# Optimization experiments

Measured on AMD Instinct MI355X. Metric: run time of the kernel, lower is better.

The kernel has to match this reference:

```python
import jax, jax.numpy as jnp
import numpy as np

B, S, D, V = 512, 64, 128, 256
NH = 4                 # sLSTM heads
HD = D // NH           # 32
INNER = 2 * D          # mLSTM inner dim (proj_factor=2.0)
NHM = 4                # mLSTM heads
DHM = INNER // NHM     # 64
BS = 4                 # qkv_proj_blocksize
NB = INNER // BS       # 64 block-diagonal qkv blocks
K = 4                  # causal conv kernel
FF = D                 # gated FFN up dim (proj_factor=1.0)


def setup_inputs():
    key = jax.random.key(0)
    ks = iter(jax.random.split(key, 40))
    def rn(shape, scale=0.02):
        return jax.random.normal(next(ks), shape, dtype=jnp.float32) * scale
    return {
        "x": jax.random.randint(next(ks), (B, S), 0, V, dtype=jnp.int32),
        "embed": rn((V, D), 0.02),
        "s_ln1": jnp.ones((2, D), jnp.float32),
        "s_gates_w": rn((2, 4, NH, HD, HD), 0.08),   # i,f,z,o headwise input projections
        "s_rec": rn((2, 4, NH, HD, HD), 0.08),       # block-diagonal recurrent kernels
        "s_bias": rn((2, 4, NH, HD), 0.1),
        "s_gn": jnp.ones((2, D), jnp.float32),
        "s_ln2": jnp.ones((2, D), jnp.float32),
        "s_ff_up": rn((2, D, 2 * FF), 0.05),
        "s_ff_down": rn((2, FF, D), 0.05),
        "m_ln1": jnp.ones((2, D), jnp.float32),
        "m_up": rn((2, D, 2 * INNER), 0.05),
        "m_conv_w": rn((2, INNER, K), 0.1),
        "m_conv_b": jnp.zeros((2, INNER), jnp.float32),
        "m_qkv_w": rn((2, 3, NB, BS, BS), 0.2),
        "m_ig_w": rn((2, 3 * INNER, NHM), 0.02),
        "m_ig_b": jnp.zeros((2, NHM), jnp.float32),
        "m_fg_w": rn((2, 3 * INNER, NHM), 0.02),
        "m_fg_b": 3.0 * jnp.ones((2, NHM), jnp.float32),
        "m_skip": jnp.ones((2, INNER), jnp.float32),
        "m_onorm": jnp.ones((2, INNER), jnp.float32),
        "m_down": rn((2, INNER, D), 0.05),
        "m_ln2": jnp.ones((2, D), jnp.float32),
        "m_ff_up": rn((2, D, 2 * FF), 0.05),
        "m_ff_down": rn((2, FF, D), 0.05),
        "post_ln": jnp.ones((D,), jnp.float32),
        "head_w": rn((D, V), 0.05),
        "head_b": jnp.zeros((V,), jnp.float32),
    }


def _ln(x, w, eps=1e-5):
    mu = x.mean(-1, keepdims=True)
    var = x.var(-1, keepdims=True)
    return (x - mu) * jax.lax.rsqrt(var + eps) * w


def _mh_ln(xh, w, eps=1e-5):
    # xh: [B,S,nh,dh]; per-head layernorm (GroupNorm), weight-only affine
    mu = xh.mean(-1, keepdims=True)
    var = xh.var(-1, keepdims=True)
    y = (xh - mu) * jax.lax.rsqrt(var + eps)
    return y * w.reshape(xh.shape[-2], xh.shape[-1])


def _ffn(x, up, down):
    g, u = jnp.split(x @ up, 2, axis=-1)
    return (jax.nn.gelu(g) * u) @ down


def _slstm(x, gw, rw, bias, gn):
    # vanilla sLSTM: stabilized exp-gated scalar-memory recurrence, block-diag recurrent kernels
    Bq, Sq, Dq = x.shape
    xh = x.reshape(Bq, Sq, NH, HD)
    # precompute input contributions for all 4 gates: [S,B,4,NH,HD]
    gx = jnp.einsum('bsnd,gned->sbgne', xh, gw) + bias

    def step(carry, g):
        h, c, n, m = carry
        raw = g + jnp.einsum('bnd,gned->bgne', h, rw)
        i_r, f_r, z_r, o_r = raw[:, 0], raw[:, 1], raw[:, 2], raw[:, 3]
        logfplusm = m + jax.nn.log_sigmoid(f_r)
        m_new = jnp.maximum(i_r, logfplusm)
        i = jnp.exp(i_r - m_new)
        f = jnp.exp(logfplusm - m_new)
        c_new = f * c + i * jnp.tanh(z_r)
        n_new = f * n + i
        h_new = jax.nn.sigmoid(o_r) * c_new / n_new
        return (h_new, c_new, n_new, m_new), h_new

    z0 = jnp.zeros((Bq, NH, HD), x.dtype)
    _, ys = jax.lax.scan(step, (z0, z0, z0, z0), gx)
    y = jnp.transpose(ys, (1, 0, 2, 3))  # [B,S,NH,HD]
    return _mh_ln(y, gn).reshape(Bq, Sq, Dq)


def _mlstm(x, up, cw, cb, qkvw, igw, igb, fgw, fgb, skip, onw, down):
    # pre-up-projection mLSTM layer with parallel stabilized matrix-memory cell
    Bq, Sq, _ = x.shape
    xm, z = jnp.split(x @ up, 2, axis=-1)  # [B,S,INNER] each
    # causal depthwise conv + swish
    conv = jax.lax.conv_general_dilated(
        xm.transpose(0, 2, 1), cw[:, None, :],
        window_strides=(1,), padding=[(K - 1, 0)], feature_group_count=INNER)
    x_conv = jax.nn.silu(conv.transpose(0, 2, 1) + cb)

    def hw(t, w):  # block-diagonal (headwise) linear, w: [NB, out, in]
        th = t.reshape(Bq, Sq, NB, BS)
        return jnp.einsum('bsni,noi->bsno', th, w).reshape(Bq, Sq, INNER)

    q = hw(x_conv, qkvw[0])
    k = hw(x_conv, qkvw[1])
    v = hw(xm, qkvw[2])

    gate_in = jnp.concatenate([q, k, v], axis=-1)          # [B,S,3*INNER]
    ig = (gate_in @ igw + igb).transpose(0, 2, 1)          # [B,NHM,S]
    fg = (gate_in @ fgw + fgb).transpose(0, 2, 1)

    qh = q.reshape(Bq, Sq, NHM, DHM).transpose(0, 2, 1, 3)  # [B,NHM,S,DHM]
    kh = k.reshape(Bq, Sq, NHM, DHM).transpose(0, 2, 1, 3)
    vh = v.reshape(Bq, Sq, NHM, DHM).transpose(0, 2, 1, 3)

    log_f = jax.nn.log_sigmoid(fg)                          # [B,NHM,S]
    c = jnp.concatenate([jnp.zeros_like(log_f[..., :1]), jnp.cumsum(log_f, -1)], -1)
    mat = c[..., 1:, None] - c[..., None, 1:]               # (i,j): sum_{t=j+1..i} log f_t
    mask = jnp.tril(jnp.ones((Sq, Sq), bool))
    log_D = jnp.where(mask, mat, -jnp.inf) + ig[..., None, :]
    max_log_D = jnp.max(log_D, -1, keepdims=True)           # [B,NHM,S,1]
    Dm = jnp.exp(log_D - max_log_D)
    qk = jnp.einsum('bhid,bhjd->bhij', qh, kh) * (DHM ** -0.5)
    Cm = qk * Dm
    norm = jnp.maximum(jnp.abs(Cm.sum(-1, keepdims=True)), jnp.exp(-max_log_D))
    Cn = Cm / (norm + 1e-6)
    h = jnp.einsum('bhij,bhjd->bhid', Cn, vh).transpose(0, 2, 1, 3)  # [B,S,NHM,DHM]
    h = _mh_ln(h, onw).reshape(Bq, Sq, INNER)
    h = (h + skip * x_conv) * jax.nn.silu(z)
    return h @ down


def _forward(x, embed, s_ln1, s_gates_w, s_rec, s_bias, s_gn, s_ln2, s_ff_up, s_ff_down,
             m_ln1, m_up, m_conv_w, m_conv_b, m_qkv_w, m_ig_w, m_ig_b, m_fg_w, m_fg_b,
             m_skip, m_onorm, m_down, m_ln2, m_ff_up, m_ff_down, post_ln, head_w, head_b):
    h = embed[x]  # [B,S,D]
    for i in range(2):
        # sLSTM block (even positions 0, 2)
        h = h + _slstm(_ln(h, s_ln1[i]), s_gates_w[i], s_rec[i], s_bias[i], s_gn[i])
        h = h + _ffn(_ln(h, s_ln2[i]), s_ff_up[i], s_ff_down[i])
        # mLSTM block (odd positions 1, 3)
        h = h + _mlstm(_ln(h, m_ln1[i]), m_up[i], m_conv_w[i], m_conv_b[i], m_qkv_w[i],
                       m_ig_w[i], m_ig_b[i], m_fg_w[i], m_fg_b[i], m_skip[i], m_onorm[i], m_down[i])
        h = h + _ffn(_ln(h, m_ln2[i]), m_ff_up[i], m_ff_down[i])
    h = _ln(h, post_ln)
    return h @ head_w + head_b


def reference(x, embed, s_ln1, s_gates_w, s_rec, s_bias, s_gn, s_ln2, s_ff_up, s_ff_down,
              m_ln1, m_up, m_conv_w, m_conv_b, m_qkv_w, m_ig_w, m_ig_b, m_fg_w, m_fg_b,
              m_skip, m_onorm, m_down, m_ln2, m_ff_up, m_ff_down, post_ln, head_w, head_b):
    return _forward(x, embed, s_ln1, s_gates_w, s_rec, s_bias, s_gn, s_ln2, s_ff_up, s_ff_down,
                    m_ln1, m_up, m_conv_w, m_conv_b, m_qkv_w, m_ig_w, m_ig_b, m_fg_w, m_fg_b,
                    m_skip, m_onorm, m_down, m_ln2, m_ff_up, m_ff_down, post_ln, head_w, head_b)
```

## Files before the change

### kernel.cpp

```cpp
#include <hip/hip_runtime.h>
#include <math.h>


__device__ __forceinline__ float sigf(float x){ return 1.f/(1.f+__expf(-x)); }
__device__ __forceinline__ float siluf(float x){ return x/(1.f+__expf(-x)); }
__device__ __forceinline__ float logsigf(float x){ return fminf(x,0.f) - log1pf(__expf(-fabsf(x))); }
__device__ __forceinline__ float geluf(float x){
  return 0.5f*x*(1.f+tanhf(0.7978845608028654f*(x+0.044715f*x*x*x)));
}
__device__ __forceinline__ void sums4(float4 v, float& s, float& q){
  s += v.x+v.y+v.z+v.w;
  q += v.x*v.x+v.y*v.y+v.z*v.z+v.w*v.w;
}

__device__ __forceinline__ void ln_rows(const float* __restrict__ src, const float* __restrict__ lnw,
                                        float* __restrict__ dst, int dstride,
                                        float (*red)[8], float (*red2)[8], int t)
{
  int r = t >> 3, l8 = t & 7;
  const float4* s4 = (const float4*)(src + (size_t)r*128 + l8*16);
  float4 v0=s4[0], v1=s4[1], v2=s4[2], v3=s4[3];
  float su=0.f, sq=0.f;
  sums4(v0,su,sq); sums4(v1,su,sq); sums4(v2,su,sq); sums4(v3,su,sq);
  red[r][l8]=su; red2[r][l8]=sq;
  __syncthreads();
  float ts=0.f, tq=0.f;
  #pragma unroll
  for (int k=0;k<8;k++){ ts+=red[r][k]; tq+=red2[r][k]; }
  float mu = ts*(1.f/128.f);
  float var = tq*(1.f/128.f) - mu*mu;
  float iv = rsqrtf(var+1e-5f);
  int c0 = l8*16;
  float vv[16];
  *(float4*)&vv[0]=v0; *(float4*)&vv[4]=v1; *(float4*)&vv[8]=v2; *(float4*)&vv[12]=v3;
  #pragma unroll
  for (int q2=0;q2<16;q2++) dst[r*dstride + c0 + q2] = (vv[q2]-mu)*iv*lnw[c0+q2];
}

__global__ __launch_bounds__(256) void k_embed(const int* __restrict__ x, const float* __restrict__ embed,
                                               float* __restrict__ h)
{
  int idx4 = blockIdx.x*256 + threadIdx.x;
  int tok = idx4 >> 5;
  int c4  = idx4 & 31;
  int id = x[tok];
  reinterpret_cast<float4*>(h)[idx4] = reinterpret_cast<const float4*>(embed)[id*32 + c4];
}

__global__ __launch_bounds__(512) void k_prep(
    const float* __restrict__ qkvw,
    const float* __restrict__ igw,
    const float* __restrict__ fgw,
    float* __restrict__ wtab)
{
  int t = threadIdx.x;
  int l = t >> 8, c = t & 255;
  int nb = c >> 2, i = c & 3;
  const float* qk  = qkvw + l*3072;
  const float* igl = igw + l*3072;
  const float* fgl = fgw + l*3072;
  float igc[4]={0,0,0,0}, igm[4]={0,0,0,0}, fgc[4]={0,0,0,0}, fgm[4]={0,0,0,0};
  #pragma unroll
  for (int o=0;o<4;o++){
    float wq = qk[nb*16 + o*4 + i];
    float wk = qk[1024 + nb*16 + o*4 + i];
    float wv = qk[2048 + nb*16 + o*4 + i];
    int no = nb*4+o;
    #pragma unroll
    for (int m=0;m<4;m++){
      igc[m] += wq*igl[no*4+m] + wk*igl[(256+no)*4+m];
      igm[m] += wv*igl[(512+no)*4+m];
      fgc[m] += wq*fgl[no*4+m] + wk*fgl[(256+no)*4+m];
      fgm[m] += wv*fgl[(512+no)*4+m];
    }
  }
  float* dst = wtab + l*4096;
  #pragma unroll
  for (int m=0;m<4;m++){
    dst[(0*256+c)*4+m] = igc[m];
    dst[(1*256+c)*4+m] = igm[m];
    dst[(2*256+c)*4+m] = fgc[m];
    dst[(3*256+c)*4+m] = fgm[m];
  }
}

__global__ __launch_bounds__(512) void k_slstm(
    float* __restrict__ h, const float* __restrict__ lnw,
    const float* __restrict__ gw, const float* __restrict__ rw,
    const float* __restrict__ bias, const float* __restrict__ gn)
{
  __shared__ float xh[64][128];
  __shared__ float hb[128];
  __shared__ float raw[512];
  __shared__ float red[64][8];
  __shared__ float red2[64][8];
  __shared__ float mu_s[64][4];
  __shared__ float iv_s[64][4];

  int t = threadIdx.x;
  int b = blockIdx.x;
  float* hrow = h + (size_t)b*8192;

  ln_rows(hrow, lnw, &xh[0][0], 128, red, red2, t);
  __syncthreads();

  int g  = t >> 7;
  int nh = (t >> 5) & 3;
  int e  = t & 31;
  float wg[32], wr[32];
  {
    const float4* g4 = (const float4*)(gw + (((g*4+nh)*32+e)*32));
    const float4* r4 = (const float4*)(rw + (((g*4+nh)*32+e)*32));
    #pragma unroll
    for (int q=0;q<8;q++){
      float4 a=g4[q]; wg[4*q]=a.x; wg[4*q+1]=a.y; wg[4*q+2]=a.z; wg[4*q+3]=a.w;
      float4 c=r4[q]; wr[4*q]=c.x; wr[4*q+1]=c.y; wr[4*q+2]=c.z; wr[4*q+3]=c.w;
    }
  }
  float bs = bias[(g*4+nh)*32+e];
  float c_s=0.f, n_s=0.f, m_s=0.f;
  if (t<128) hb[t]=0.f;
  __syncthreads();

  for (int s=0;s<64;s++){
    const float4* xr = (const float4*)&xh[s][nh*32];
    const float4* hr = (const float4*)&hb[nh*32];
    float acc = bs;
    #pragma unroll
    for (int q=0;q<8;q++){
      float4 xv = xr[q]; float4 hv = hr[q];
      acc += xv.x*wg[4*q+0] + xv.y*wg[4*q+1] + xv.z*wg[4*q+2] + xv.w*wg[4*q+3];
      acc += hv.x*wr[4*q+0] + hv.y*wr[4*q+1] + hv.z*wr[4*q+2] + hv.w*wr[4*q+3];
    }
    raw[t] = acc;
    __syncthreads();
    if (t < 128){
      float i_r = raw[t], f_r = raw[128+t], z_r = raw[256+t], o_r = raw[384+t];
      float lf = m_s + logsigf(f_r);
      float mn = fmaxf(i_r, lf);
      float iv = __expf(i_r-mn), fv = __expf(lf-mn);
      c_s = fv*c_s + iv*tanhf(z_r);
      n_s = fv*n_s + iv;
      m_s = mn;
      float hn = sigf(o_r)*c_s/n_s;
      hb[t] = hn;
      xh[s][t] = hn;
    }
    __syncthreads();
  }

  if (t < 256){
    int s = t>>2, n = t&3;
    const float4* yr = (const float4*)&xh[s][n*32];
    float su=0.f, sq=0.f;
    #pragma unroll
    for (int q=0;q<8;q++){ float4 v = yr[q]; sums4(v,su,sq); }
    float mu = su*(1.f/32.f);
    float var = sq*(1.f/32.f) - mu*mu;
    mu_s[s][n]=mu; iv_s[s][n]=rsqrtf(var+1e-5f);
  }
  __syncthreads();
  #pragma unroll
  for (int rr=0; rr<16; rr++){
    int idx = t + 512*rr;
    int s = idx>>7, c = idx&127;
    float y = (xh[s][c] - mu_s[s][c>>5]) * iv_s[s][c>>5] * gn[c];
    hrow[idx] += y;
  }
}

__global__ __launch_bounds__(256) void k_ffn(
    float* __restrict__ h, const float* __restrict__ lnw,
    const float* __restrict__ up, const float* __restrict__ down)
{
  __shared__ float xln[32][132];
  __shared__ float hid[32][132];
  __shared__ float bws[2][16][256];
  __shared__ float red[32][8];
  __shared__ float red2[32][8];
  int t = threadIdx.x;
  size_t tok0 = (size_t)blockIdx.x * 32;

  ln_rows(h + tok0*128, lnw, &xln[0][0], 132, red, red2, t);
  __syncthreads();

  int r0 = (t >> 5) * 4;
  int c0 = (t & 31) * 4;

  {
    float4 regs[4];
    auto stage = [&](int kc){
      #pragma unroll
      for (int j=0;j<4;j++){
        int idx = t + 256*j;
        int row = idx >> 6, c4 = idx & 63;
        regs[j] = *(const float4*)(up + (size_t)(kc*16+row)*256 + c4*4);
      }
    };
    auto wrt = [&](int buf){
      #pragma unroll
      for (int j=0;j<4;j++){
        int idx = t + 256*j;
        int row = idx >> 6, c4 = idx & 63;
        *(float4*)&bws[buf][row][c4*4] = regs[j];
      }
    };
    stage(0); wrt(0);
    __syncthreads();
    float4 ag[4], au[4];
    #pragma unroll
    for (int i=0;i<4;i++){ ag[i]=make_float4(0,0,0,0); au[i]=make_float4(0,0,0,0); }
    for (int kc=0;kc<8;kc++){
      if (kc<7) stage(kc+1);
      int buf = kc & 1;
      #pragma unroll
      for (int k=0;k<16;k++){
        float4 wg = *(float4*)&bws[buf][k][c0];
        float4 wu = *(float4*)&bws[buf][k][c0+128];
        int kk = kc*16 + k;
        #pragma unroll
        for (int i=0;i<4;i++){
          float xv = xln[r0+i][kk];
          ag[i].x+=xv*wg.x; ag[i].y+=xv*wg.y; ag[i].z+=xv*wg.z; ag[i].w+=xv*wg.w;
          au[i].x+=xv*wu.x; au[i].y+=xv*wu.y; au[i].z+=xv*wu.z; au[i].w+=xv*wu.w;
        }
      }
      if (kc<7) wrt(buf^1);
      __syncthreads();
    }
    #pragma unroll
    for (int i=0;i<4;i++){
      hid[r0+i][c0+0] = geluf(ag[i].x)*au[i].x;
      hid[r0+i][c0+1] = geluf(ag[i].y)*au[i].y;
      hid[r0+i][c0+2] = geluf(ag[i].z)*au[i].z;
      hid[r0+i][c0+3] = geluf(ag[i].w)*au[i].w;
    }
  }
  __syncthreads();

  {
    float (*bw2)[16][128] = (float (*)[16][128])bws;
    float4 regs[2];
    auto stage = [&](int kc){
      #pragma unroll
      for (int j=0;j<2;j++){
        int idx = t + 256*j;
        int row = idx >> 5, c4 = idx & 31;
        regs[j] = *(const float4*)(down + (size_t)(kc*16+row)*128 + c4*4);
      }
    };
    auto wrt = [&](int buf){
      #pragma unroll
      for (int j=0;j<2;j++){
        int idx = t + 256*j;
        int row = idx >> 5, c4 = idx & 31;
        *(float4*)&bw2[buf][row][c4*4] = regs[j];
      }
    };
    stage(0); wrt(0);
    __syncthreads();
    float4 a2[4];
    #pragma unroll
    for (int i=0;i<4;i++) a2[i]=make_float4(0,0,0,0);
    for (int kc=0;kc<8;kc++){
      if (kc<7) stage(kc+1);
      int buf = kc & 1;
      #pragma unroll
      for (int k=0;k<16;k++){
        float4 wv = *(float4*)&bw2[buf][k][c0];
        int kk = kc*16 + k;
        #pragma unroll
        for (int i=0;i<4;i++){
          float xv = hid[r0+i][kk];
          a2[i].x+=xv*wv.x; a2[i].y+=xv*wv.y; a2[i].z+=xv*wv.z; a2[i].w+=xv*wv.w;
        }
      }
      if (kc<7) wrt(buf^1);
      __syncthreads();
    }
    #pragma unroll
    for (int i=0;i<4;i++){
      float* dstp = h + (tok0 + r0 + i)*128 + c0;
      float4 hv = *(float4*)dstp;
      hv.x += a2[i].x; hv.y += a2[i].y; hv.z += a2[i].z; hv.w += a2[i].w;
      *(float4*)dstp = hv;
    }
  }
}

__global__ __launch_bounds__(256) void k_up(
    const float* __restrict__ h, const float* __restrict__ lnw,
    const float* __restrict__ up, float* __restrict__ xm, float* __restrict__ z)
{
  __shared__ float xln[64][132];
  __shared__ float bw[2][32][128];
  __shared__ float red[64][4];
  __shared__ float red2[64][4];
  int t = threadIdx.x;
  int mt = blockIdx.x >> 2, nt = blockIdx.x & 3;
  size_t tok0 = (size_t)mt * 64;
  int n0 = nt * 128;

  {
    int r = t >> 2, l = t & 3;
    const float4* s4 = (const float4*)(h + (tok0 + (size_t)r)*128 + l*32);
    float4 v[8];
    float su=0.f, sq=0.f;
    #pragma unroll
    for (int q=0;q<8;q++){ v[q]=s4[q]; sums4(v[q],su,sq); }
    red[r][l]=su; red2[r][l]=sq;
    __syncthreads();
    float ts=red[r][0]+red[r][1]+red[r][2]+red[r][3];
    float tq=red2[r][0]+red2[r][1]+red2[r][2]+red2[r][3];
    float mu=ts*(1.f/128.f);
    float var=tq*(1.f/128.f)-mu*mu;
    float iv=rsqrtf(var+1e-5f);
    int cb=l*32;
    #pragma unroll
    for (int q=0;q<8;q++){
      xln[r][cb+q*4+0]=(v[q].x-mu)*iv*lnw[cb+q*4+0];
      xln[r][cb+q*4+1]=(v[q].y-mu)*iv*lnw[cb+q*4+1];
      xln[r][cb+q*4+2]=(v[q].z-mu)*iv*lnw[cb+q*4+2];
      xln[r][cb+q*4+3]=(v[q].w-mu)*iv*lnw[cb+q*4+3];
    }
  }

  float4 regs[4];
  auto stage = [&](int kc){
    #pragma unroll
    for (int j=0;j<4;j++){
      int idx = t + 256*j;
      int row = idx >> 5, c4 = idx & 31;
      regs[j] = *(const float4*)(up + (size_t)(kc*32+row)*512 + n0 + c4*4);
    }
  };
  auto wrt = [&](int buf){
    #pragma unroll
    for (int j=0;j<4;j++){
      int idx = t + 256*j;
      int row = idx >> 5, c4 = idx & 31;
      *(float4*)&bw[buf][row][c4*4] = regs[j];
    }
  };
  stage(0); wrt(0);
  __syncthreads();

  int r0 = (t >> 5) * 8;
  int c0 = (t & 31) * 4;
  float4 acc4[8];
  #pragma unroll
  for (int i=0;i<8;i++) acc4[i]=make_float4(0,0,0,0);

  for (int kc=0;kc<4;kc++){
    if (kc<3) stage(kc+1);
    int buf = kc & 1;
    #pragma unroll 8
    for (int k=0;k<32;k++){
      float4 wv = *(float4*)&bw[buf][k][c0];
      int kk = kc*32 + k;
      #pragma unroll
      for (int i=0;i<8;i++){
        float xv = xln[r0+i][kk];
        acc4[i].x += xv*wv.x; acc4[i].y += xv*wv.y; acc4[i].z += xv*wv.z; acc4[i].w += xv*wv.w;
      }
    }
    if (kc<3) wrt(buf^1);
    __syncthreads();
  }

  float* dst; int cbase;
  if (n0 < 256){ dst = xm; cbase = n0 + c0; }
  else         { dst = z;  cbase = n0 - 256 + c0; }
  #pragma unroll
  for (int i=0;i<8;i++)
    *(float4*)(dst + (tok0 + r0 + i)*256 + cbase) = acc4[i];
}

__global__ __launch_bounds__(256) void k_convgates(
    const float* __restrict__ xm, float* __restrict__ xc,
    const float* __restrict__ cw, const float* __restrict__ cb,
    const float* __restrict__ wtab,
    const float* __restrict__ igb, const float* __restrict__ fgb,
    float* __restrict__ ig, float* __restrict__ fg)
{
  int t = threadIdx.x;
  int b = blockIdx.x;
  int c4 = t & 63, sr = t >> 6;
  int c0 = c4*4;
  const float* src = xm + (size_t)b*16384;
  float* dstc = xc + (size_t)b*16384;

  float4 r0 = *(const float4*)(cw + (c0+0)*4);
  float4 r1 = *(const float4*)(cw + (c0+1)*4);
  float4 r2 = *(const float4*)(cw + (c0+2)*4);
  float4 r3 = *(const float4*)(cw + (c0+3)*4);
  float4 wk0 = make_float4(r0.x, r1.x, r2.x, r3.x);
  float4 wk1 = make_float4(r0.y, r1.y, r2.y, r3.y);
  float4 wk2 = make_float4(r0.z, r1.z, r2.z, r3.z);
  float4 wk3 = make_float4(r0.w, r1.w, r2.w, r3.w);
  float4 bias4 = *(const float4*)(cb + c0);

  float4 Wigc[4], Wigm[4], Wfgc[4], Wfgm[4];
  #pragma unroll
  for (int i=0;i<4;i++){
    Wigc[i] = *(const float4*)(wtab + (0*256+c0+i)*4);
    Wigm[i] = *(const float4*)(wtab + (1*256+c0+i)*4);
    Wfgc[i] = *(const float4*)(wtab + (2*256+c0+i)*4);
    Wfgm[i] = *(const float4*)(wtab + (3*256+c0+i)*4);
  }

  int s0 = sr*16;
  float4 w0 = make_float4(0,0,0,0), w1 = w0, w2 = w0;
  if (s0 >= 3){
    w0 = *(const float4*)(src + (size_t)(s0-3)*256 + c0);
    w1 = *(const float4*)(src + (size_t)(s0-2)*256 + c0);
    w2 = *(const float4*)(src + (size_t)(s0-1)*256 + c0);
  }

  for (int j=0;j<16;j++){
    int s = s0 + j;
    float4 w3 = *(const float4*)(src + (size_t)s*256 + c0);
    float4 a;
    a.x = bias4.x + w0.x*wk0.x + w1.x*wk1.x + w2.x*wk2.x + w3.x*wk3.x;
    a.y = bias4.y + w0.y*wk0.y + w1.y*wk1.y + w2.y*wk2.y + w3.y*wk3.y;
    a.z = bias4.z + w0.z*wk0.z + w1.z*wk1.z + w2.z*wk2.z + w3.z*wk3.z;
    a.w = bias4.w + w0.w*wk0.w + w1.w*wk1.w + w2.w*wk2.w + w3.w*wk3.w;
    a.x = siluf(a.x); a.y = siluf(a.y); a.z = siluf(a.z); a.w = siluf(a.w);
    *(float4*)(dstc + (size_t)s*256 + c0) = a;

    float pig[4] = {0.f,0.f,0.f,0.f};
    float pfg[4] = {0.f,0.f,0.f,0.f};
    const float xcv[4] = {a.x,a.y,a.z,a.w};
    const float xmv[4] = {w3.x,w3.y,w3.z,w3.w};
    #pragma unroll
    for (int i=0;i<4;i++){
      pig[0] += xcv[i]*Wigc[i].x + xmv[i]*Wigm[i].x;
      pig[1] += xcv[i]*Wigc[i].y + xmv[i]*Wigm[i].y;
      pig[2] += xcv[i]*Wigc[i].z + xmv[i]*Wigm[i].z;
      pig[3] += xcv[i]*Wigc[i].w + xmv[i]*Wigm[i].w;
      pfg[0] += xcv[i]*Wfgc[i].x + xmv[i]*Wfgm[i].x;
      pfg[1] += xcv[i]*Wfgc[i].y + xmv[i]*Wfgm[i].y;
      pfg[2] += xcv[i]*Wfgc[i].z + xmv[i]*Wfgm[i].z;
      pfg[3] += xcv[i]*Wfgc[i].w + xmv[i]*Wfgm[i].w;
    }
    #pragma unroll
    for (int off=32; off>=1; off>>=1){
      #pragma unroll
      for (int m=0;m<4;m++){
        pig[m] += __shfl_xor(pig[m], off, 64);
        pfg[m] += __shfl_xor(pfg[m], off, 64);
      }
    }
    if (c4 == 0){
      #pragma unroll
      for (int m=0;m<4;m++){
        ig[(size_t)b*256 + m*64 + s] = pig[m] + igb[m];
        fg[(size_t)b*256 + m*64 + s] = pfg[m] + fgb[m];
      }
    }
    w0=w1; w1=w2; w2=w3;
  }
}

__global__ __launch_bounds__(256) void k_attn(
    float* __restrict__ xm, const float* __restrict__ xc,
    const float* __restrict__ qkvw,
    const float* __restrict__ igp, const float* __restrict__ fgp,
    const float* __restrict__ onorm)
{
  __shared__ float qs[64][68];
  __shared__ float ksm[64][68];
  __shared__ float vsm[64][68];
  __shared__ float xcl[64][68];
  __shared__ float xml[64][68];
  __shared__ float cnm[64][65];
  __shared__ float csum[65];
  __shared__ float pmax[64];
  __shared__ float igl[64];
  __shared__ float lfs[64];
  __shared__ float nrec[64];

  int t = threadIdx.x;
  int b = blockIdx.x >> 2, hh = blockIdx.x & 3;
  const float* xcb = xc + (size_t)b*16384 + hh*64;
  float* xmb = xm + (size_t)b*16384 + hh*64;

  #pragma unroll
  for (int j=0;j<4;j++){
    int u = t + 256*j;
    int r = u >> 4, q4 = u & 15;
    *(float4*)&xcl[r][q4*4] = *(const float4*)(xcb + (size_t)r*256 + q4*4);
    *(float4*)&xml[r][q4*4] = *(const float4*)(xmb + (size_t)r*256 + q4*4);
  }
  if (t < 64){
    lfs[t] = logsigf(fgp[(size_t)b*256 + hh*64 + t]);
    igl[t] = igp[(size_t)b*256 + hh*64 + t];
  }
  __syncthreads();
  if (t == 0){
    float cacc = 0.f, pm = -1e30f;
    csum[0] = 0.f;
    for (int s=0;s<64;s++){
      cacc += lfs[s];
      csum[s+1] = cacc;
      pm = fmaxf(pm, igl[s] - cacc);
      pmax[s] = pm;
    }
  }
  #pragma unroll
  for (int j=0;j<4;j++){
    int u = t + 256*j;
    int s = u >> 4, lb = u & 15;
    int nb = hh*16 + lb;
    const float* xq = &xcl[s][lb*4];
    const float* xv = &xml[s][lb*4];
    #pragma unroll
    for (int o=0;o<4;o++){
      float4 wq = *(const float4*)(qkvw + nb*16 + o*4);
      float4 wkk = *(const float4*)(qkvw + 1024 + nb*16 + o*4);
      float4 wv = *(const float4*)(qkvw + 2048 + nb*16 + o*4);
      qs[s][lb*4+o]  = wq.x*xq[0]+wq.y*xq[1]+wq.z*xq[2]+wq.w*xq[3];
      ksm[s][lb*4+o] = wkk.x*xq[0]+wkk.y*xq[1]+wkk.z*xq[2]+wkk.w*xq[3];
      vsm[s][lb*4+o] = wv.x*xv[0]+wv.y*xv[1]+wv.z*xv[2]+wv.w*xv[3];
    }
  }
  __syncthreads();

  int i = t >> 2;
  int jq = t & 3;
  float mi = csum[i+1] + pmax[i];
  float rs = 0.f;
  for (int jj=0;jj<16;jj++){
    int j = jq*16 + jj;
    if (j <= i){
      const float4* qa = (const float4*)&qs[i][0];
      const float4* ka = (const float4*)&ksm[j][0];
      float dp = 0.f;
      #pragma unroll
      for (int kk=0;kk<16;kk++){
        float4 a = qa[kk], c = ka[kk];
        dp += a.x*c.x + a.y*c.y + a.z*c.z + a.w*c.w;
      }
      float val = dp * 0.125f * __expf(csum[i+1] - csum[j+1] + igl[j] - mi);
      cnm[i][j] = val;
      rs += val;
    }
  }
  rs += __shfl_xor(rs, 1, 4);
  rs += __shfl_xor(rs, 2, 4);
  if (jq == 0){
    float nm = fmaxf(fabsf(rs), __expf(-mi));
    nrec[i] = 1.f/(nm + 1e-6f);
  }
  __syncthreads();

  int d0 = jq*16;
  float acc[16];
  #pragma unroll
  for (int q=0;q<16;q++) acc[q]=0.f;
  float nr = nrec[i];
  for (int j=0;j<=i;j++){
    float cwv = cnm[i][j] * nr;
    const float4* va = (const float4*)&vsm[j][d0];
    #pragma unroll
    for (int q=0;q<4;q++){
      float4 v4 = va[q];
      acc[q*4+0] += cwv*v4.x; acc[q*4+1] += cwv*v4.y; acc[q*4+2] += cwv*v4.z; acc[q*4+3] += cwv*v4.w;
    }
  }
  float su=0.f, sq=0.f;
  #pragma unroll
  for (int q=0;q<16;q++){ su += acc[q]; sq += acc[q]*acc[q]; }
  su += __shfl_xor(su,1,4); su += __shfl_xor(su,2,4);
  sq += __shfl_xor(sq,1,4); sq += __shfl_xor(sq,2,4);
  float mu = su*(1.f/64.f);
  float var = sq*(1.f/64.f) - mu*mu;
  float ivr = rsqrtf(var + 1e-5f);
  const float* onw = onorm + hh*64 + d0;
  #pragma unroll
  for (int q=0;q<4;q++){
    float4 o4;
    o4.x = (acc[q*4+0]-mu)*ivr*onw[q*4+0];
    o4.y = (acc[q*4+1]-mu)*ivr*onw[q*4+1];
    o4.z = (acc[q*4+2]-mu)*ivr*onw[q*4+2];
    o4.w = (acc[q*4+3]-mu)*ivr*onw[q*4+3];
    *(float4*)(xmb + (size_t)i*256 + d0 + q*4) = o4;
  }
}

__global__ __launch_bounds__(256) void k_comb_down(
    float* __restrict__ h, const float* __restrict__ hln,
    const float* __restrict__ xc, const float* __restrict__ z,
    const float* __restrict__ skip, const float* __restrict__ down)
{
  __shared__ float comb[32][260];
  __shared__ float bw[2][16][128];
  int t = threadIdx.x;
  size_t tok0 = (size_t)blockIdx.x*32;
  #pragma unroll
  for (int j=0;j<8;j++){
    int f4 = t + 256*j;
    int r = f4 >> 6, c4 = f4 & 63;
    size_t gi = (tok0 + r)*256 + c4*4;
    float4 a  = *(const float4*)(hln + gi);
    float4 xv = *(const float4*)(xc + gi);
    float4 zv = *(const float4*)(z + gi);
    float4 sk = *(const float4*)(skip + c4*4);
    float4 o;
    o.x = (a.x + sk.x*xv.x)*siluf(zv.x);
    o.y = (a.y + sk.y*xv.y)*siluf(zv.y);
    o.z = (a.z + sk.z*xv.z)*siluf(zv.z);
    o.w = (a.w + sk.w*xv.w)*siluf(zv.w);
    *(float4*)&comb[r][c4*4] = o;
  }

  float4 regs[2];
  auto stage = [&](int kc){
    #pragma unroll
    for (int j=0;j<2;j++){
      int idx = t + 256*j;
      int row = idx >> 5, c4 = idx & 31;
      regs[j] = *(const float4*)(down + (size_t)(kc*16+row)*128 + c4*4);
    }
  };
  auto wrt = [&](int buf){
    #pragma unroll
    for (int j=0;j<2;j++){
      int idx = t + 256*j;
      int row = idx >> 5, c4 = idx & 31;
      *(float4*)&bw[buf][row][c4*4] = regs[j];
    }
  };
  stage(0); wrt(0);
  __syncthreads();

  int r0 = (t >> 5) * 4;
  int c0 = (t & 31) * 4;
  float4 a2[4];
  #pragma unroll
  for (int i=0;i<4;i++) a2[i]=make_float4(0,0,0,0);
  for (int kc=0;kc<16;kc++){
    if (kc<15) stage(kc+1);
    int buf = kc & 1;
    #pragma unroll
    for (int k=0;k<16;k++){
      float4 wv = *(float4*)&bw[buf][k][c0];
      int kk = kc*16 + k;
      #pragma unroll
      for (int i=0;i<4;i++){
        float xv = comb[r0+i][kk];
        a2[i].x+=xv*wv.x; a2[i].y+=xv*wv.y; a2[i].z+=xv*wv.z; a2[i].w+=xv*wv.w;
      }
    }
    if (kc<15) wrt(buf^1);
    __syncthreads();
  }
  #pragma unroll
  for (int i=0;i<4;i++){
    float* dstp = h + (tok0 + r0 + i)*128 + c0;
    float4 hv = *(float4*)dstp;
    hv.x += a2[i].x; hv.y += a2[i].y; hv.z += a2[i].z; hv.w += a2[i].w;
    *(float4*)dstp = hv;
  }
}

__global__ __launch_bounds__(256) void k_head(
    const float* __restrict__ h, const float* __restrict__ lnw,
    const float* __restrict__ w, const float* __restrict__ bias2,
    float* __restrict__ out)
{
  __shared__ float xln[32][132];
  __shared__ float bws[2][16][256];
  __shared__ float red[32][8];
  __shared__ float red2[32][8];
  int t = threadIdx.x;
  size_t tok0 = (size_t)blockIdx.x * 32;

  ln_rows(h + tok0*128, lnw, &xln[0][0], 132, red, red2, t);
  __syncthreads();

  float4 regs[4];
  auto stage = [&](int kc){
    #pragma unroll
    for (int j=0;j<4;j++){
      int idx = t + 256*j;
      int row = idx >> 6, c4 = idx & 63;
      regs[j] = *(const float4*)(w + (size_t)(kc*16+row)*256 + c4*4);
    }
  };
  auto wrt = [&](int buf){
    #pragma unroll
    for (int j=0;j<4;j++){
      int idx = t + 256*j;
      int row = idx >> 6, c4 = idx & 63;
      *(float4*)&bws[buf][row][c4*4] = regs[j];
    }
  };
  stage(0); wrt(0);
  __syncthreads();

  int r0 = (t >> 5) * 4;
  int c0 = (t & 31) * 8;
  float4 a0[4], a1[4];
  #pragma unroll
  for (int i=0;i<4;i++){ a0[i]=make_float4(0,0,0,0); a1[i]=make_float4(0,0,0,0); }
  for (int kc=0;kc<8;kc++){
    if (kc<7) stage(kc+1);
    int buf = kc & 1;
    #pragma unroll
    for (int k=0;k<16;k++){
      float4 w0 = *(float4*)&bws[buf][k][c0];
      float4 w1 = *(float4*)&bws[buf][k][c0+4];
      int kk = kc*16 + k;
      #pragma unroll
      for (int i=0;i<4;i++){
        float xv = xln[r0+i][kk];
        a0[i].x+=xv*w0.x; a0[i].y+=xv*w0.y; a0[i].z+=xv*w0.z; a0[i].w+=xv*w0.w;
        a1[i].x+=xv*w1.x; a1[i].y+=xv*w1.y; a1[i].z+=xv*w1.z; a1[i].w+=xv*w1.w;
      }
    }
    if (kc<7) wrt(buf^1);
    __syncthreads();
  }
  float4 b0 = *(const float4*)(bias2 + c0);
  float4 b1 = *(const float4*)(bias2 + c0 + 4);
  #pragma unroll
  for (int i=0;i<4;i++){
    float* dstp = out + (tok0 + r0 + i)*256 + c0;
    float4 o0, o1;
    o0.x=a0[i].x+b0.x; o0.y=a0[i].y+b0.y; o0.z=a0[i].z+b0.z; o0.w=a0[i].w+b0.w;
    o1.x=a1[i].x+b1.x; o1.y=a1[i].y+b1.y; o1.z=a1[i].z+b1.z; o1.w=a1[i].w+b1.w;
    ((float4*)dstp)[0]=o0; ((float4*)dstp)[1]=o1;
  }
}

extern "C" void kernel_launch(void* const* d_in, const int* in_sizes, int n_in,
                              void* d_out, int out_size, void* d_ws, size_t ws_size,
                              hipStream_t stream)
{
  const int*   x      = (const int*)  d_in[0];
  const float* embed  = (const float*)d_in[1];
  const float* s_ln1  = (const float*)d_in[2];
  const float* s_gw   = (const float*)d_in[3];
  const float* s_rec  = (const float*)d_in[4];
  const float* s_bias = (const float*)d_in[5];
  const float* s_gn   = (const float*)d_in[6];
  const float* s_ln2  = (const float*)d_in[7];
  const float* s_ffu  = (const float*)d_in[8];
  const float* s_ffd  = (const float*)d_in[9];
  const float* m_ln1  = (const float*)d_in[10];
  const float* m_up   = (const float*)d_in[11];
  const float* m_cw   = (const float*)d_in[12];
  const float* m_cb   = (const float*)d_in[13];
  const float* m_qkv  = (const float*)d_in[14];
  const float* m_igw  = (const float*)d_in[15];
  const float* m_igb  = (const float*)d_in[16];
  const float* m_fgw  = (const float*)d_in[17];
  const float* m_fgb  = (const float*)d_in[18];
  const float* m_skip = (const float*)d_in[19];
  const float* m_onw  = (const float*)d_in[20];
  const float* m_down = (const float*)d_in[21];
  const float* m_ln2  = (const float*)d_in[22];
  const float* m_ffu  = (const float*)d_in[23];
  const float* m_ffd  = (const float*)d_in[24];
  const float* postln = (const float*)d_in[25];
  const float* headw  = (const float*)d_in[26];
  const float* headb  = (const float*)d_in[27];

  float* p = (float*)d_ws;
  float* hbuf = p; p += 4194304;
  size_t avail = ws_size / 4;
  const size_t need_full = 4194304ULL + 3ULL*8388608ULL + 2ULL*131072ULL + 8192ULL;
  float* xmbuf;
  if (avail >= need_full){ xmbuf = p; p += 8388608; }
  else                   { xmbuf = (float*)d_out; }
  float* zbuf  = p; p += 8388608;
  float* xcbuf = p; p += 8388608;
  float* igbuf = p; p += 131072;
  float* fgbuf = p; p += 131072;
  float* wtab  = p; p += 8192;

  k_prep<<<1, 512, 0, stream>>>(m_qkv, m_igw, m_fgw, wtab);
  k_embed<<<4096, 256, 0, stream>>>(x, embed, hbuf);

  for (int i=0;i<2;i++){
    k_slstm<<<512, 512, 0, stream>>>(hbuf, s_ln1+i*128, s_gw+i*16384, s_rec+i*16384,
                                     s_bias+i*512, s_gn+i*128);
    k_ffn<<<1024, 256, 0, stream>>>(hbuf, s_ln2+i*128, s_ffu+i*32768, s_ffd+i*16384);
    k_up<<<2048, 256, 0, stream>>>(hbuf, m_ln1+i*128, m_up+i*65536, xmbuf, zbuf);
    k_convgates<<<512, 256, 0, stream>>>(xmbuf, xcbuf, m_cw+i*1024, m_cb+i*256,
                                         wtab+i*4096, m_igb+i*4, m_fgb+i*4,
                                         igbuf, fgbuf);
    k_attn<<<2048, 256, 0, stream>>>(xmbuf, xcbuf, m_qkv+i*3072, igbuf, fgbuf, m_onw+i*256);
    k_comb_down<<<1024, 256, 0, stream>>>(hbuf, xmbuf, xcbuf, zbuf, m_skip+i*256, m_down+i*32768);
    k_ffn<<<1024, 256, 0, stream>>>(hbuf, m_ln2+i*128, m_ffu+i*32768, m_ffd+i*16384);
  }

  k_head<<<1024, 256, 0, stream>>>(hbuf, postln, headw, headb, (float*)d_out);
}
```

Baseline: 1.349 ms.

## Drop x staging in attention, hoist qkv weights and q row into registers

```diff
diff --git a/kernel.cpp b/kernel.cpp
--- a/kernel.cpp
+++ b/kernel.cpp
@@ -471,8 +471,6 @@
   __shared__ float qs[64][68];
   __shared__ float ksm[64][68];
   __shared__ float vsm[64][68];
-  __shared__ float xcl[64][68];
-  __shared__ float xml[64][68];
   __shared__ float cnm[64][65];
   __shared__ float csum[65];
   __shared__ float pmax[64];
@@ -485,18 +483,22 @@
   const float* xcb = xc + (size_t)b*16384 + hh*64;
   float* xmb = xm + (size_t)b*16384 + hh*64;
 
-  #pragma unroll
-  for (int j=0;j<4;j++){
-    int u = t + 256*j;
-    int r = u >> 4, q4 = u & 15;
-    *(float4*)&xcl[r][q4*4] = *(const float4*)(xcb + (size_t)r*256 + q4*4);
-    *(float4*)&xml[r][q4*4] = *(const float4*)(xmb + (size_t)r*256 + q4*4);
-  }
   if (t < 64){
     lfs[t] = logsigf(fgp[(size_t)b*256 + hh*64 + t]);
     igl[t] = igp[(size_t)b*256 + hh*64 + t];
   }
   __syncthreads();
+
+  int lb = t & 15;
+  int nb = hh*16 + lb;
+  float4 wq[4], wk[4], wv[4];
+  #pragma unroll
+  for (int o=0;o<4;o++){
+    wq[o] = *(const float4*)(qkvw + nb*16 + o*4);
+    wk[o] = *(const float4*)(qkvw + 1024 + nb*16 + o*4);
+    wv[o] = *(const float4*)(qkvw + 2048 + nb*16 + o*4);
+  }
+
   if (t == 0){
     float cacc = 0.f, pm = -1e30f;
     csum[0] = 0.f;
@@ -507,38 +509,49 @@
       pmax[s] = pm;
     }
   }
+
   #pragma unroll
   for (int j=0;j<4;j++){
-    int u = t + 256*j;
-    int s = u >> 4, lb = u & 15;
-    int nb = hh*16 + lb;
-    const float* xq = &xcl[s][lb*4];
-    const float* xv = &xml[s][lb*4];
-    #pragma unroll
-    for (int o=0;o<4;o++){
-      float4 wq = *(const float4*)(qkvw + nb*16 + o*4);
-      float4 wkk = *(const float4*)(qkvw + 1024 + nb*16 + o*4);
-      float4 wv = *(const float4*)(qkvw + 2048 + nb*16 + o*4);
-      qs[s][lb*4+o]  = wq.x*xq[0]+wq.y*xq[1]+wq.z*xq[2]+wq.w*xq[3];
-      ksm[s][lb*4+o] = wkk.x*xq[0]+wkk.y*xq[1]+wkk.z*xq[2]+wkk.w*xq[3];
-      vsm[s][lb*4+o] = wv.x*xv[0]+wv.y*xv[1]+wv.z*xv[2]+wv.w*xv[3];
-    }
+    int s = (t >> 4) + j*16;
+    float4 x4 = *(const float4*)(xcb + (size_t)s*256 + lb*4);
+    float4 m4 = *(const float4*)(xmb + (size_t)s*256 + lb*4);
+    float4 qv, kv, vv;
+    qv.x = wq[0].x*x4.x + wq[0].y*x4.y + wq[0].z*x4.z + wq[0].w*x4.w;
+    qv.y = wq[1].x*x4.x + wq[1].y*x4.y + wq[1].z*x4.z + wq[1].w*x4.w;
+    qv.z = wq[2].x*x4.x + wq[2].y*x4.y + wq[2].z*x4.z + wq[2].w*x4.w;
+    qv.w = wq[3].x*x4.x + wq[3].y*x4.y + wq[3].z*x4.z + wq[3].w*x4.w;
+    kv.x = wk[0].x*x4.x + wk[0].y*x4.y + wk[0].z*x4.z + wk[0].w*x4.w;
+    kv.y = wk[1].x*x4.x + wk[1].y*x4.y + wk[1].z*x4.z + wk[1].w*x4.w;
+    kv.z = wk[2].x*x4.x + wk[2].y*x4.y + wk[2].z*x4.z + wk[2].w*x4.w;
+    kv.w = wk[3].x*x4.x + wk[3].y*x4.y + wk[3].z*x4.z + wk[3].w*x4.w;
+    vv.x = wv[0].x*m4.x + wv[0].y*m4.y + wv[0].z*m4.z + wv[0].w*m4.w;
+    vv.y = wv[1].x*m4.x + wv[1].y*m4.y + wv[1].z*m4.z + wv[1].w*m4.w;
+    vv.z = wv[2].x*m4.x + wv[2].y*m4.y + wv[2].z*m4.z + wv[2].w*m4.w;
+    vv.w = wv[3].x*m4.x + wv[3].y*m4.y + wv[3].z*m4.z + wv[3].w*m4.w;
+    *(float4*)&qs[s][lb*4]  = qv;
+    *(float4*)&ksm[s][lb*4] = kv;
+    *(float4*)&vsm[s][lb*4] = vv;
   }
   __syncthreads();
 
   int i = t >> 2;
   int jq = t & 3;
   float mi = csum[i+1] + pmax[i];
+
+  float4 ql[16];
+  #pragma unroll
+  for (int kk=0;kk<16;kk++) ql[kk] = *(float4*)&qs[i][kk*4];
+
+  int iwmax = ((t & ~63) >> 2) + 15;
   float rs = 0.f;
-  for (int jj=0;jj<16;jj++){
-    int j = jq*16 + jj;
+  for (int jj=0; jq + jj*4 <= iwmax && jj < 16; jj++){
+    int j = jq + jj*4;
     if (j <= i){
-      const float4* qa = (const float4*)&qs[i][0];
       const float4* ka = (const float4*)&ksm[j][0];
       float dp = 0.f;
       #pragma unroll
       for (int kk=0;kk<16;kk++){
-        float4 a = qa[kk], c = ka[kk];
+        float4 a = ql[kk], c = ka[kk];
         dp += a.x*c.x + a.y*c.y + a.z*c.z + a.w*c.w;
       }
       float val = dp * 0.125f * __expf(csum[i+1] - csum[j+1] + igl[j] - mi);
```

After: 1.167 ms. -13.5%, faster.
